# Optimization experiments

Measured on AMD Instinct MI355X. Metric: run time of the kernel, lower is better.

The kernel has to match this reference:

```python
import jax, jax.numpy as jnp
import numpy as np

WIN = 7            # skimage default win_size
K1 = 0.01
K2 = 0.03
DATA_RANGE = 1.0   # images are in [0, 1]
PAD = (WIN - 1) // 2


def _uniform_filter_valid(x):
    # x: [N, 1, H, W] -> valid 7x7 box filter (== skimage uniform_filter cropped by PAD)
    k = jnp.ones((1, 1, WIN, WIN), x.dtype) / (WIN * WIN)
    return jax.lax.conv_general_dilated(
        x, k, window_strides=(1, 1), padding='VALID',
        dimension_numbers=('NCHW', 'OIHW', 'NCHW'))


def _ssim_mean(a, b):
    # a, b: [B, C, H, W]; each [H, W] slice is one independent SSIM image
    B, C, H, W = a.shape
    x = a.reshape(B * C, 1, H, W)
    y = b.reshape(B * C, 1, H, W)

    ux = _uniform_filter_valid(x)
    uy = _uniform_filter_valid(y)
    uxx = _uniform_filter_valid(x * x)
    uyy = _uniform_filter_valid(y * y)
    uxy = _uniform_filter_valid(x * y)

    NP = WIN * WIN
    cov_norm = NP / (NP - 1.0)  # sample covariance correction (skimage default)
    vx = cov_norm * (uxx - ux * ux)
    vy = cov_norm * (uyy - uy * uy)
    vxy = cov_norm * (uxy - ux * uy)

    C1 = (K1 * DATA_RANGE) ** 2
    C2 = (K2 * DATA_RANGE) ** 2

    S = ((2.0 * ux * uy + C1) * (2.0 * vxy + C2)) / \
        ((ux * ux + uy * uy + C1) * (vx + vy + C2))

    # skimage crops PAD border then means; VALID conv already cropped it.
    # All images are the same size, so np.average(per-image means) == global mean.
    return jnp.mean(S)


def setup_inputs() -> dict:
    key = jax.random.key(0)
    k1, k2 = jax.random.split(key)
    pred = jax.random.uniform(k1, (32, 4, 384, 384), dtype=jnp.float32)
    actual = jax.random.uniform(k2, (32, 4, 384, 384), dtype=jnp.float32)
    return {"pred": pred, "actual": actual}


def reference(pred, actual):
    return _ssim_mean(pred, actual)
```

## Files before the change

### kernel.cpp

```cpp
#include <hip/hip_runtime.h>


#define H 384
#define W 384
#define OWIDTH 378
#define NIMG 128
#define CH 7
#define P2 394
#define PLANE (CH * P2)
#define SY 49
#define NSTRIP 8
#define NBLK (NSTRIP * NIMG)
#define NGRP 48
#define NSLOT (NGRP * CH)

__device__ __forceinline__ float wave_reduce(float v) {
#pragma unroll
    for (int off = 32; off > 0; off >>= 1) v += __shfl_down(v, off, 64);
    return v;
}

#define VSTEP(SLOT, LR, XN, YN) do {                                      \
    const float xo = xv[SLOT], yo = yv[SLOT];                             \
    const float xn = (XN), yn = (YN);                                     \
    sx += xn - xo; sy += yn - yo;                                         \
    sq = fmaf(xn, xn, fmaf(yn, yn, fmaf(-xo, xo, fmaf(-yo, yo, sq))));    \
    sxy = fmaf(xn, yn, fmaf(-xo, yo, sxy));                               \
    xv[SLOT] = xn; yv[SLOT] = yn;                                         \
    stA[(LR) * P2 + t] = make_float2(sx, sy);                             \
    stB[(LR) * P2 + t] = make_float2(sq, sxy);                            \
} while (0)

__global__ __launch_bounds__(384, 5) void ssim_main(const float* __restrict__ pred,
                                                    const float* __restrict__ act,
                                                    float* __restrict__ partials) {
    __shared__ __align__(16) float2 st[2 * PLANE];
    __shared__ float red[6];

    const int t = threadIdx.x;
    const int y0 = blockIdx.x * SY;
    const int nrows = (blockIdx.x == NSTRIP - 1) ? (OWIDTH - (NSTRIP - 1) * SY) : SY;
    const int nch = nrows / CH;
    const size_t base = (size_t)blockIdx.y * (H * W);

    float2* const stA = st;
    float2* const stB = st + PLANE;

    const float* xp = pred + base + (size_t)y0 * W + t;
    const float* ap = act  + base + (size_t)y0 * W + t;

    const int g = t / 7;
    const int r = t - 7 * g;
    const int c0 = g * 8;
    const int nmax = OWIDTH - c0;
    const float C1B = 0.2401f;
    const float C2B = 2.1168f;
    float acc = 0.f;

    float xv[7], yv[7];
    float sx = 0.f, sy = 0.f, sq = 0.f, sxy = 0.f;
#pragma unroll
    for (int i = 0; i < 7; ++i) {
        xv[i] = xp[i * W];
        yv[i] = ap[i * W];
    }
#pragma unroll
    for (int i = 0; i < 7; ++i) {
        sx += xv[i]; sy += yv[i];
        sq = fmaf(xv[i], xv[i], fmaf(yv[i], yv[i], sq));
        sxy = fmaf(xv[i], yv[i], sxy);
    }
    stA[t] = make_float2(sx, sy);
    stB[t] = make_float2(sq, sxy);
    {
        float nx[6], ny[6];
#pragma unroll
        for (int i = 0; i < 6; ++i) {
            nx[i] = xp[(7 + i) * W];
            ny[i] = ap[(7 + i) * W];
        }
#pragma unroll
        for (int i = 1; i < 7; ++i) VSTEP(i - 1, i, nx[i - 1], ny[i - 1]);
    }

    int c = 0;
    while (true) {
        __syncthreads();
        if (t < NSLOT) {
            const float4* qa = (const float4*)(stA + r * P2 + c0);
            float4 a[8];
#pragma unroll
            for (int k = 0; k < 8; ++k) a[k] = qa[k];
            float vx[16], vy[16];
#pragma unroll
            for (int k = 0; k < 8; ++k) {
                vx[2 * k]     = a[k].x; vy[2 * k]     = a[k].y;
                vx[2 * k + 1] = a[k].z; vy[2 * k + 1] = a[k].w;
            }
            float S0[8], S1[8];
            float sA = ((vx[0] + vx[1]) + (vx[2] + vx[3])) + ((vx[4] + vx[5]) + vx[6]);
            float sB = ((vy[0] + vy[1]) + (vy[2] + vy[3])) + ((vy[4] + vy[5]) + vy[6]);
            S0[0] = sA; S1[0] = sB;
#pragma unroll
            for (int j = 1; j < 8; ++j) {
                sA += vx[j + 6] - vx[j - 1]; S0[j] = sA;
                sB += vy[j + 6] - vy[j - 1]; S1[j] = sB;
            }
            const float4* qb = (const float4*)(stB + r * P2 + c0);
            float4 b[8];
#pragma unroll
            for (int k = 0; k < 8; ++k) b[k] = qb[k];
            float vq[16], vw[16];
#pragma unroll
            for (int k = 0; k < 8; ++k) {
                vq[2 * k]     = b[k].x; vw[2 * k]     = b[k].y;
                vq[2 * k + 1] = b[k].z; vw[2 * k + 1] = b[k].w;
            }
            float s2 = ((vq[0] + vq[1]) + (vq[2] + vq[3])) + ((vq[4] + vq[5]) + vq[6]);
            float s3 = ((vw[0] + vw[1]) + (vw[2] + vw[3])) + ((vw[4] + vw[5]) + vw[6]);
#pragma unroll
            for (int j = 0; j < 8; ++j) {
                if (j) {
                    s2 += vq[j + 6] - vq[j - 1];
                    s3 += vw[j + 6] - vw[j - 1];
                }
                const float Sx = S0[j], Sy = S1[j];
                const float Sq = s2, Sxy = s3;
                const float p  = Sx * Sy;
                const float qq = fmaf(Sx, Sx, Sy * Sy);
                const float n1 = fmaf(2.f, p, C1B);
                const float n2 = fmaf(98.f, Sxy, fmaf(-2.f, p, C2B));
                const float d1 = qq + C1B;
                const float d2 = fmaf(49.f, Sq, C2B - qq);
                const float s  = (n1 * n2) * __builtin_amdgcn_rcpf(d1 * d2);
                acc = (j < nmax) ? acc + s : acc;
            }
        }
        if (++c == nch) break;
        __syncthreads();
        {
            const int rb = 7 * c + 6;
            float nx[7], ny[7];
#pragma unroll
            for (int i = 0; i < 7; ++i) {
                nx[i] = xp[(rb + i) * W];
                ny[i] = ap[(rb + i) * W];
            }
            VSTEP(6, 0, nx[0], ny[0]);
            VSTEP(0, 1, nx[1], ny[1]);
            VSTEP(1, 2, nx[2], ny[2]);
            VSTEP(2, 3, nx[3], ny[3]);
            VSTEP(3, 4, nx[4], ny[4]);
            VSTEP(4, 5, nx[5], ny[5]);
            VSTEP(5, 6, nx[6], ny[6]);
        }
    }

    const float wsum = wave_reduce(acc);
    if ((t & 63) == 0) red[t >> 6] = wsum;
    __syncthreads();
    if (t == 0) {
        partials[blockIdx.x + NSTRIP * blockIdx.y] =
            ((red[0] + red[1]) + (red[2] + red[3])) + (red[4] + red[5]);
    }
}

__global__ __launch_bounds__(1024) void ssim_finalize(const float* __restrict__ partials,
                                                      float* __restrict__ out) {
    __shared__ double red[1024];
    const int t = threadIdx.x;
    double s = 0.0;
    for (int i = t; i < NBLK; i += 1024) s += (double)partials[i];
    red[t] = s;
    __syncthreads();
#pragma unroll
    for (int off = 512; off > 0; off >>= 1) {
        if (t < off) red[t] += red[t + off];
        __syncthreads();
    }
    if (t == 0) out[0] = (float)(red[0] / ((double)NIMG * OWIDTH * OWIDTH));
}

extern "C" void kernel_launch(void* const* d_in, const int* in_sizes, int n_in,
                              void* d_out, int out_size, void* d_ws, size_t ws_size,
                              hipStream_t stream) {
    const float* pred = (const float*)d_in[0];
    const float* act  = (const float*)d_in[1];
    float* partials = (float*)d_ws;
    dim3 grid(NSTRIP, NIMG);
    ssim_main<<<grid, 384, 0, stream>>>(pred, act, partials);
    ssim_finalize<<<1, 1024, 0, stream>>>(partials, (float*)d_out);
}
```

Baseline: 178.7 us.

## Retile SSIM into 18-row strips with 6-row chunks and prefetched loads

Splits each image into 21 strips of 18 output rows instead of 8 strips of 49 rows, so there are more blocks and better load balance across CUs. Each block runs exactly three fully unrolled 6-row chunks. Each thread's horizontal pass now covers 6 columns instead of 8, which removes the column-bound predicate, and all 378 slots are mapped with a new row/group indexing. Global loads for the next chunk are issued before the barrier and horizontal pass so they overlap with compute. In exchange, each strip re-reads its 6-row vertical halo, which adds global memory traffic.

Measured after the change: 169.5 us. 5.1% less time.

```diff
diff --git a/kernel.cpp b/kernel.cpp
--- a/kernel.cpp
+++ b/kernel.cpp
@@ -5,13 +5,13 @@
 #define W 384
 #define OWIDTH 378
 #define NIMG 128
-#define CH 7
-#define P2 394
+#define CH 6
+#define P2 386
 #define PLANE (CH * P2)
-#define SY 49
-#define NSTRIP 8
+#define SY 18
+#define NSTRIP 21
 #define NBLK (NSTRIP * NIMG)
-#define NGRP 48
+#define NGRP 63
 #define NSLOT (NGRP * CH)
 
 __device__ __forceinline__ float wave_reduce(float v) {
@@ -31,6 +31,53 @@
     stB[(LR) * P2 + t] = make_float2(sq, sxy);                            \
 } while (0)
 
+#define HORIZ do {                                                              \
+    if (t < NSLOT) {                                                            \
+        const float4* qa = (const float4*)(stA + hoff);                         \
+        const float4 a0 = qa[0], a1 = qa[1], a2 = qa[2],                        \
+                     a3 = qa[3], a4 = qa[4], a5 = qa[5];                        \
+        const float vx[12] = {a0.x, a0.z, a1.x, a1.z, a2.x, a2.z,               \
+                              a3.x, a3.z, a4.x, a4.z, a5.x, a5.z};              \
+        const float vy[12] = {a0.y, a0.w, a1.y, a1.w, a2.y, a2.w,               \
+                              a3.y, a3.w, a4.y, a4.w, a5.y, a5.w};              \
+        float S0[6], S1[6];                                                     \
+        float sA = ((vx[0] + vx[1]) + (vx[2] + vx[3])) + ((vx[4] + vx[5]) + vx[6]); \
+        float sB = ((vy[0] + vy[1]) + (vy[2] + vy[3])) + ((vy[4] + vy[5]) + vy[6]); \
+        S0[0] = sA; S1[0] = sB;                                                 \
+        _Pragma("unroll")                                                       \
+        for (int j = 1; j < 6; ++j) {                                           \
+            sA += vx[j + 6] - vx[j - 1]; S0[j] = sA;                            \
+            sB += vy[j + 6] - vy[j - 1]; S1[j] = sB;                            \
+        }                                                                       \
+        const float4* qb = (const float4*)(stB + hoff);                         \
+        const float4 b0 = qb[0], b1 = qb[1], b2 = qb[2],                        \
+                     b3 = qb[3], b4 = qb[4], b5 = qb[5];                        \
+        const float vq[12] = {b0.x, b0.z, b1.x, b1.z, b2.x, b2.z,               \
+                              b3.x, b3.z, b4.x, b4.z, b5.x, b5.z};              \
+        const float vw[12] = {b0.y, b0.w, b1.y, b1.w, b2.y, b2.w,               \
+                              b3.y, b3.w, b4.y, b4.w, b5.y, b5.w};              \
+        float s2 = ((vq[0] + vq[1]) + (vq[2] + vq[3])) + ((vq[4] + vq[5]) + vq[6]); \
+        float s3 = ((vw[0] + vw[1]) + (vw[2] + vw[3])) + ((vw[4] + vw[5]) + vw[6]); \
+        _Pragma("unroll")                                                       \
+        for (int j = 0; j < 6; ++j) {                                           \
+            if (j) {                                                            \
+                s2 += vq[j + 6] - vq[j - 1];                                    \
+                s3 += vw[j + 6] - vw[j - 1];                                    \
+            }                                                                   \
+            const float Sx = S0[j], Sy = S1[j];                                 \
+            const float Sq = s2, Sxy = s3;                                      \
+            const float p  = Sx * Sy;                                           \
+            const float qq = fmaf(Sx, Sx, Sy * Sy);                             \
+            const float n1 = fmaf(2.f, p, C1B);                                 \
+            const float n2 = fmaf(98.f, Sxy, fmaf(-2.f, p, C2B));               \
+            const float d1 = qq + C1B;                                          \
+            const float d2 = fmaf(49.f, Sq, C2B - qq);                          \
+            const float s  = (n1 * n2) * __builtin_amdgcn_rcpf(d1 * d2);        \
+            acc += s;                                                           \
+        }                                                                       \
+    }                                                                           \
+} while (0)
+
 __global__ __launch_bounds__(384, 5) void ssim_main(const float* __restrict__ pred,
                                                     const float* __restrict__ act,
                                                     float* __restrict__ partials) {
@@ -39,8 +86,6 @@
 
     const int t = threadIdx.x;
     const int y0 = blockIdx.x * SY;
-    const int nrows = (blockIdx.x == NSTRIP - 1) ? (OWIDTH - (NSTRIP - 1) * SY) : SY;
-    const int nch = nrows / CH;
     const size_t base = (size_t)blockIdx.y * (H * W);
 
     float2* const stA = st;
@@ -49,21 +94,23 @@
     const float* xp = pred + base + (size_t)y0 * W + t;
     const float* ap = act  + base + (size_t)y0 * W + t;
 
-    const int g = t / 7;
-    const int r = t - 7 * g;
-    const int c0 = g * 8;
-    const int nmax = OWIDTH - c0;
+    const int r = t / NGRP;
+    const int g = t - NGRP * r;
+    const int hoff = r * P2 + 6 * g;
     const float C1B = 0.2401f;
     const float C2B = 2.1168f;
     float acc = 0.f;
 
+    float xr[12], yr[12];
+#pragma unroll
+    for (int i = 0; i < 12; ++i) {
+        xr[i] = xp[i * W];
+        yr[i] = ap[i * W];
+    }
     float xv[7], yv[7];
+#pragma unroll
+    for (int i = 0; i < 7; ++i) { xv[i] = xr[i]; yv[i] = yr[i]; }
     float sx = 0.f, sy = 0.f, sq = 0.f, sxy = 0.f;
-#pragma unroll
-    for (int i = 0; i < 7; ++i) {
-        xv[i] = xp[i * W];
-        yv[i] = ap[i * W];
-    }
 #pragma unroll
     for (int i = 0; i < 7; ++i) {
         sx += xv[i]; sy += yv[i];
@@ -72,89 +119,50 @@
     }
     stA[t] = make_float2(sx, sy);
     stB[t] = make_float2(sq, sxy);
+    VSTEP(0, 1, xr[7],  yr[7]);
+    VSTEP(1, 2, xr[8],  yr[8]);
+    VSTEP(2, 3, xr[9],  yr[9]);
+    VSTEP(3, 4, xr[10], yr[10]);
+    VSTEP(4, 5, xr[11], yr[11]);
+
     {
-        float nx[6], ny[6];
+        float pfx[6], pfy[6];
 #pragma unroll
         for (int i = 0; i < 6; ++i) {
-            nx[i] = xp[(7 + i) * W];
-            ny[i] = ap[(7 + i) * W];
+            pfx[i] = xp[(12 + i) * W];
+            pfy[i] = ap[(12 + i) * W];
         }
-#pragma unroll
-        for (int i = 1; i < 7; ++i) VSTEP(i - 1, i, nx[i - 1], ny[i - 1]);
-    }
-
-    int c = 0;
-    while (true) {
-        __syncthreads();
-        if (t < NSLOT) {
-            const float4* qa = (const float4*)(stA + r * P2 + c0);
-            float4 a[8];
-#pragma unroll
-            for (int k = 0; k < 8; ++k) a[k] = qa[k];
-            float vx[16], vy[16];
-#pragma unroll
-            for (int k = 0; k < 8; ++k) {
-                vx[2 * k]     = a[k].x; vy[2 * k]     = a[k].y;
-                vx[2 * k + 1] = a[k].z; vy[2 * k + 1] = a[k].w;
-            }
-            float S0[8], S1[8];
-            float sA = ((vx[0] + vx[1]) + (vx[2] + vx[3])) + ((vx[4] + vx[5]) + vx[6]);
-            float sB = ((vy[0] + vy[1]) + (vy[2] + vy[3])) + ((vy[4] + vy[5]) + vy[6]);
-            S0[0] = sA; S1[0] = sB;
-#pragma unroll
-            for (int j = 1; j < 8; ++j) {
-                sA += vx[j + 6] - vx[j - 1]; S0[j] = sA;
-                sB += vy[j + 6] - vy[j - 1]; S1[j] = sB;
-            }
-            const float4* qb = (const float4*)(stB + r * P2 + c0);
-            float4 b[8];
-#pragma unroll
-            for (int k = 0; k < 8; ++k) b[k] = qb[k];
-            float vq[16], vw[16];
-#pragma unroll
-            for (int k = 0; k < 8; ++k) {
-                vq[2 * k]     = b[k].x; vw[2 * k]     = b[k].y;
-                vq[2 * k + 1] = b[k].z; vw[2 * k + 1] = b[k].w;
-            }
-            float s2 = ((vq[0] + vq[1]) + (vq[2] + vq[3])) + ((vq[4] + vq[5]) + vq[6]);
-            float s3 = ((vw[0] + vw[1]) + (vw[2] + vw[3])) + ((vw[4] + vw[5]) + vw[6]);
-#pragma unroll
-            for (int j = 0; j < 8; ++j) {
-                if (j) {
-                    s2 += vq[j + 6] - vq[j - 1];
-                    s3 += vw[j + 6] - vw[j - 1];
-                }
-                const float Sx = S0[j], Sy = S1[j];
-                const float Sq = s2, Sxy = s3;
-                const float p  = Sx * Sy;
-                const float qq = fmaf(Sx, Sx, Sy * Sy);
-                const float n1 = fmaf(2.f, p, C1B);
-                const float n2 = fmaf(98.f, Sxy, fmaf(-2.f, p, C2B));
-                const float d1 = qq + C1B;
-                const float d2 = fmaf(49.f, Sq, C2B - qq);
-                const float s  = (n1 * n2) * __builtin_amdgcn_rcpf(d1 * d2);
-                acc = (j < nmax) ? acc + s : acc;
-            }
+        __syncthreads();
+        HORIZ;
+        __syncthreads();
+        VSTEP(5, 0, pfx[0], pfy[0]);
+        VSTEP(6, 1, pfx[1], pfy[1]);
+        VSTEP(0, 2, pfx[2], pfy[2]);
+        VSTEP(1, 3, pfx[3], pfy[3]);
+        VSTEP(2, 4, pfx[4], pfy[4]);
+        VSTEP(3, 5, pfx[5], pfy[5]);
+    }
+
+    {
+        float pfx[6], pfy[6];
+#pragma unroll
+        for (int i = 0; i < 6; ++i) {
+            pfx[i] = xp[(18 + i) * W];
+            pfy[i] = ap[(18 + i) * W];
         }
-        if (++c == nch) break;
-        __syncthreads();
-        {
-            const int rb = 7 * c + 6;
-            float nx[7], ny[7];
-#pragma unroll
-            for (int i = 0; i < 7; ++i) {
-                nx[i] = xp[(rb + i) * W];
-                ny[i] = ap[(rb + i) * W];
-            }
-            VSTEP(6, 0, nx[0], ny[0]);
-            VSTEP(0, 1, nx[1], ny[1]);
-            VSTEP(1, 2, nx[2], ny[2]);
-            VSTEP(2, 3, nx[3], ny[3]);
-            VSTEP(3, 4, nx[4], ny[4]);
-            VSTEP(4, 5, nx[5], ny[5]);
-            VSTEP(5, 6, nx[6], ny[6]);
-        }
-    }
+        __syncthreads();
+        HORIZ;
+        __syncthreads();
+        VSTEP(4, 0, pfx[0], pfy[0]);
+        VSTEP(5, 1, pfx[1], pfy[1]);
+        VSTEP(6, 2, pfx[2], pfy[2]);
+        VSTEP(0, 3, pfx[3], pfy[3]);
+        VSTEP(1, 4, pfx[4], pfy[4]);
+        VSTEP(2, 5, pfx[5], pfy[5]);
+    }
+
+    __syncthreads();
+    HORIZ;
 
     const float wsum = wave_reduce(acc);
     if ((t & 63) == 0) red[t >> 6] = wsum;
```
